# Performance work log

Hardware: AMD Instinct MI355X
Metric: run time of the kernel (lower is better)

The kernel has to match this reference:

```python
import jax, jax.numpy as jnp
import numpy as np

TEMP = 0.07  # softmax temperature T


def _l2norm(x, axis=1, eps=1e-12):
    return x / jnp.clip(jnp.linalg.norm(x, axis=axis, keepdims=True), eps, None)


def setup_inputs() -> dict:
    key = jax.random.key(0)
    k1, k2, k3, k4 = jax.random.split(key, 4)
    B, K, D = 256, 8192, 128
    q = jax.random.normal(k1, (B, D), dtype=jnp.float32)
    ba_queue = _l2norm(jax.random.normal(k2, (K, D), dtype=jnp.float32))
    nonba_queue = _l2norm(jax.random.normal(k3, (K, D), dtype=jnp.float32))
    targets = jax.random.randint(k4, (B,), 0, 2, dtype=jnp.int64)
    return {"q": q, "ba_queue": ba_queue, "nonba_queue": nonba_queue, "targets": targets}


def reference(q, ba_queue, nonba_queue, targets):
    K = ba_queue.shape[0]
    # encoder output is L2-normalized; queues are detached buffers
    qn = _l2norm(q, axis=1)
    all_feature = jnp.concatenate([qn, ba_queue, nonba_queue], axis=0)  # [N, D]
    all_label = jnp.concatenate([
        targets.astype(jnp.int32),
        jnp.ones((K,), dtype=jnp.int32),
        jnp.zeros((K,), dtype=jnp.int32),
    ])  # [N]
    N = all_feature.shape[0]

    # [N, N] similarity logits
    sim = jnp.matmul(all_feature, all_feature.T) / TEMP
    logits = sim - jax.lax.stop_gradient(jnp.max(sim, axis=1, keepdims=True))

    # positive mask (same label), excluding self
    mask = (all_label[:, None] == all_label[None, :]).astype(jnp.float32)
    logits_mask = 1.0 - jnp.eye(N, dtype=jnp.float32)
    mask = mask * logits_mask

    exp_logits = jnp.exp(logits) * logits_mask
    log_prob = logits - jnp.log(jnp.sum(exp_logits, axis=1, keepdims=True))
    mean_log_prob_pos = jnp.sum(mask * log_prob, axis=1) / jnp.sum(mask, axis=1)
    return -jnp.mean(mean_log_prob_pos)
```

## Files before the change

### kernel.cpp

```cpp
#include <hip/hip_runtime.h>
#include <hip/hip_bf16.h>
#include <stdint.h>

#define TEMPERATURE 0.07f
#define SC 20.6099312f

constexpr int NQ = 256;
constexpr int KQ = 8192;
constexpr int D  = 128;
constexpr int N  = NQ + 2 * KQ;
constexpr int CS = 26;
constexpr int BN = 128;
constexpr int NT = N / BN;
constexpr int RBM = N / 128;
constexpr int RBF = N / 256;

typedef float f32x16 __attribute__((ext_vector_type(16)));
typedef long  l64x2  __attribute__((ext_vector_type(2)));

constexpr size_t OFF_F32  = 0;
constexpr size_t OFF_8P   = OFF_F32  + (size_t)N * D * 4;
constexpr size_t OFF_8S   = OFF_8P   + (size_t)N * D;
constexpr size_t OFF_DIAG = OFF_8S   + (size_t)N * D;
constexpr size_t OFF_PART = OFF_DIAG + (size_t)N * 4;
constexpr size_t OFF_LP   = OFF_PART + (size_t)CS * N * 4;
constexpr size_t OFF_S    = OFF_LP   + (size_t)260 * 2 * 128 * 4;
constexpr size_t OFF_CNT  = OFF_S    + 2 * 128 * 4;
constexpr size_t OFF_BSUM = OFF_CNT  + 16;

__global__ __launch_bounds__(256) void k_prep(const float* __restrict__ q,
                                              const float* __restrict__ ba,
                                              const float* __restrict__ nb,
                                              const long long* __restrict__ tgt,
                                              float* __restrict__ ff,
                                              unsigned char* __restrict__ fb8p,
                                              unsigned char* __restrict__ fb8s,
                                              float* __restrict__ diag,
                                              float* __restrict__ lp) {
    __shared__ float red[4][2][128];
    int wid = threadIdx.x >> 6, lane = threadIdx.x & 63;
    int rbase = blockIdx.x * 64 + wid * 16;
    int slot = ((lane >> 2) & 1) * 4 + (lane >> 4);
    int poff = slot * 16 + ((lane >> 3) & 1) * 8 + (lane & 3) * 2;
    float s0x = 0.f, s0y = 0.f, s1x = 0.f, s1y = 0.f;
    for (int i = 0; i < 16; ++i) {
        int r = rbase + i;
        const float* src = (r < NQ) ? (q + (size_t)r * D)
                         : (r < NQ + KQ) ? (ba + (size_t)(r - NQ) * D)
                         : (nb + (size_t)(r - NQ - KQ) * D);
        float2 v = *(const float2*)(src + lane * 2);
        float a = v.x, b = v.y;
        int lab;
        if (r < NQ) {
            float ss = a * a + b * b;
            #pragma unroll
            for (int m = 1; m < 64; m <<= 1) ss += __shfl_xor(ss, m);
            float scale = 1.0f / fmaxf(sqrtf(ss), 1e-12f);
            a *= scale; b *= scale;
            lab = (int)tgt[r];
        } else {
            lab = (r < NQ + KQ) ? 1 : 0;
        }
        *(float2*)(ff + (size_t)r * D + lane * 2) = make_float2(a, b);
        int w8  = __builtin_amdgcn_cvt_pk_fp8_f32(a, b, 0, false);
        int w8s = __builtin_amdgcn_cvt_pk_fp8_f32(a * SC, b * SC, 0, false);
        *(unsigned short*)(fb8p + (size_t)r * D + poff)     = (unsigned short)w8;
        *(unsigned short*)(fb8s + (size_t)r * D + lane * 2) = (unsigned short)w8s;
        float dd = __builtin_amdgcn_cvt_f32_fp8(w8, 0) * __builtin_amdgcn_cvt_f32_fp8(w8s, 0)
                 + __builtin_amdgcn_cvt_f32_fp8(w8, 1) * __builtin_amdgcn_cvt_f32_fp8(w8s, 1);
        #pragma unroll
        for (int m = 1; m < 64; m <<= 1) dd += __shfl_xor(dd, m);
        if (lane == 0) diag[r] = __builtin_amdgcn_exp2f(dd - SC);
        if (lab) { s1x += a; s1y += b; } else { s0x += a; s0y += b; }
    }
    red[wid][0][lane * 2]     = s0x;
    red[wid][0][lane * 2 + 1] = s0y;
    red[wid][1][lane * 2]     = s1x;
    red[wid][1][lane * 2 + 1] = s1y;
    __syncthreads();
    int lab2 = threadIdx.x >> 7, d = threadIdx.x & 127;
    float s = red[0][lab2][d] + red[1][lab2][d] + red[2][lab2][d] + red[3][lab2][d];
    lp[((size_t)blockIdx.x * 2 + lab2) * 128 + d] = s;
}

__global__ __launch_bounds__(256) void k_lsum_b(const float* __restrict__ lp,
                                                const long long* __restrict__ tgt,
                                                float* __restrict__ S,
                                                int* __restrict__ cnt) {
    int lab = threadIdx.x >> 7;
    int d   = threadIdx.x & 127;
    float s[4] = {0.f, 0.f, 0.f, 0.f};
    for (int b = 0; b < 260; b += 4) {
        #pragma unroll
        for (int j = 0; j < 4; ++j)
            s[j] += lp[((size_t)(b + j) * 2 + lab) * 128 + d];
    }
    S[lab * 128 + d] = (s[0] + s[1]) + (s[2] + s[3]);
    if (threadIdx.x < 64) {
        int c = 0;
        #pragma unroll
        for (int i = 0; i < 4; ++i) c += (int)tgt[threadIdx.x + 64 * i];
        #pragma unroll
        for (int m = 1; m < 64; m <<= 1) c += __shfl_xor(c, m);
        if (threadIdx.x == 0) { cnt[0] = (NQ - c) + KQ; cnt[1] = c + KQ; }
    }
}

__global__ __launch_bounds__(256, 4) void k_main(const unsigned char* __restrict__ fb8p,
                                                 const unsigned char* __restrict__ fb8s,
                                                 float* __restrict__ part) {
    __shared__ __align__(16) unsigned char lds[2][BN * 128];
    const int bid = blockIdx.x;
    const int rb = bid / CS, cs = bid % CS;
    const int tid = threadIdx.x;
    const int lane = tid & 63;
    const int wid  = tid >> 6;
    const int l31 = lane & 31, lhi = lane >> 5;
    const int rw = rb * 128 + wid * 32;

    int soff[4], dstoff[4];
    #pragma unroll
    for (int i = 0; i < 4; ++i) {
        int crow = wid * 32 + i * 8 + (lane >> 3);
        soff[i]   = crow * 128 + (((lane & 7) ^ (crow & 7)) << 4);
        dstoff[i] = (wid * 4 + i) * 1024 + (lane & 63) * 16;
    }

    long rf[8];
    #pragma unroll
    for (int ks = 0; ks < 8; ++ks)
        rf[ks] = *(const long*)(fb8s + (size_t)(rw + l31) * D + ks * 16 + lhi * 8);

    float rsum = 0.f;

    {
        const unsigned char* base = fb8p + (size_t)cs * (BN * 128);
        #pragma unroll
        for (int i = 0; i < 4; ++i)
            __builtin_amdgcn_global_load_lds(
                (const __attribute__((address_space(1))) unsigned int*)(base + soff[i]),
                (__attribute__((address_space(3))) unsigned int*)(&lds[0][dstoff[i]]),
                16, 0, 0);
    }
    asm volatile("s_waitcnt vmcnt(0)" ::: "memory");
    __builtin_amdgcn_s_barrier();

    int cur = 0;
    for (int t = 0; t < 5; ++t) {
        int ct = cs + t * CS;

        if (t + 1 < 5) {
            const unsigned char* base = fb8p + ((size_t)ct + CS) * (BN * 128);
            #pragma unroll
            for (int i = 0; i < 4; ++i)
                __builtin_amdgcn_global_load_lds(
                    (const __attribute__((address_space(1))) unsigned int*)(base + soff[i]),
                    (__attribute__((address_space(3))) unsigned int*)(&lds[cur ^ 1][dstoff[i]]),
                    16, 0, 0);
        }

        f32x16 acc[4];
        #pragma unroll
        for (int i = 0; i < 4; ++i)
            #pragma unroll
            for (int e = 0; e < 16; ++e) acc[i][e] = -SC;

        __builtin_amdgcn_s_setprio(1);
        #pragma unroll
        for (int ks2 = 0; ks2 < 4; ++ks2) {
            #pragma unroll
            for (int cc = 0; cc < 4; ++cc) {
                int crow = cc * 32 + l31;
                l64x2 cf = *(const l64x2*)(&lds[cur][crow * 128 +
                               ((((lhi << 2) + ks2) ^ (crow & 7)) << 4)]);
                acc[cc] = __builtin_amdgcn_mfma_f32_32x32x16_fp8_fp8(cf.x, rf[ks2 * 2],     acc[cc], 0, 0, 0);
                acc[cc] = __builtin_amdgcn_mfma_f32_32x32x16_fp8_fp8(cf.y, rf[ks2 * 2 + 1], acc[cc], 0, 0, 0);
            }
        }
        __builtin_amdgcn_s_setprio(0);

        #pragma unroll
        for (int cc = 0; cc < 4; ++cc) {
            float p = 0.f;
            #pragma unroll
            for (int g = 0; g < 16; ++g)
                p += __builtin_amdgcn_exp2f(acc[cc][g]);
            rsum += p;
        }

        asm volatile("s_waitcnt vmcnt(0)" ::: "memory");
        __builtin_amdgcn_s_barrier();
        cur ^= 1;
    }

    rsum += __shfl_xor(rsum, 32);
    if (lane < 32)
        part[(size_t)cs * N + rw + lane] = rsum;
}

__global__ __launch_bounds__(256) void k_rowfin(const float* __restrict__ part,
                                                const float* __restrict__ ff,
                                                const float* __restrict__ S,
                                                const float* __restrict__ diag,
                                                const int* __restrict__ cnt,
                                                const long long* __restrict__ tgt,
                                                float* __restrict__ bsum) {
    __shared__ float sS[256];
    __shared__ float red[256];
    sS[threadIdx.x] = S[threadIdx.x];
    __syncthreads();
    int r = blockIdx.x * 256 + threadIdx.x;
    float se = 0.f;
    #pragma unroll
    for (int c = 0; c < CS; ++c) se += part[(size_t)c * N + r];
    se -= diag[r];
    float lse = logf(se) + 1.0f / TEMPERATURE;
    int lab = (r < NQ) ? (int)tgt[r] : ((r < NQ + KQ) ? 1 : 0);
    const float4* frow = (const float4*)(ff + (size_t)r * D);
    const float4* srow = (const float4*)(sS + lab * 128);
    float dS = 0.f;
    #pragma unroll
    for (int i = 0; i < 32; ++i) {
        float4 f = frow[i];
        float4 s = srow[i];
        dS += f.x * s.x + f.y * s.y + f.z * s.z + f.w * s.w;
    }
    float P = (float)(cnt[lab] - 1);
    float mlpp = (dS - 1.0f) / (TEMPERATURE * P) - lse;
    red[threadIdx.x] = mlpp;
    __syncthreads();
    for (int s2 = 128; s2 > 0; s2 >>= 1) {
        if (threadIdx.x < s2) red[threadIdx.x] += red[threadIdx.x + s2];
        __syncthreads();
    }
    if (threadIdx.x == 0) bsum[blockIdx.x] = red[0];
}

__global__ __launch_bounds__(64) void k_final(const float* __restrict__ bsum,
                                              float* __restrict__ out) {
    float s = bsum[threadIdx.x];
    if (threadIdx.x == 0) s += bsum[64];
    #pragma unroll
    for (int m = 1; m < 64; m <<= 1) s += __shfl_xor(s, m);
    if (threadIdx.x == 0) out[0] = -s / (float)N;
}

extern "C" void kernel_launch(void* const* d_in, const int* in_sizes, int n_in,
                              void* d_out, int out_size, void* d_ws, size_t ws_size,
                              hipStream_t stream) {
    const float* q       = (const float*)d_in[0];
    const float* ba      = (const float*)d_in[1];
    const float* nb      = (const float*)d_in[2];
    const long long* tgt = (const long long*)d_in[3];
    char* ws = (char*)d_ws;
    float*         ff   = (float*)(ws + OFF_F32);
    unsigned char* fb8p = (unsigned char*)(ws + OFF_8P);
    unsigned char* fb8s = (unsigned char*)(ws + OFF_8S);
    float*         diag = (float*)(ws + OFF_DIAG);
    float*         part = (float*)(ws + OFF_PART);
    float*         lp   = (float*)(ws + OFF_LP);
    float*         S    = (float*)(ws + OFF_S);
    int*           cnt  = (int*)(ws + OFF_CNT);
    float*         bsum = (float*)(ws + OFF_BSUM);

    k_prep  <<<260,      256, 0, stream>>>(q, ba, nb, tgt, ff, fb8p, fb8s, diag, lp);
    k_lsum_b<<<1,        256, 0, stream>>>(lp, tgt, S, cnt);
    k_main  <<<RBM * CS, 256, 0, stream>>>(fb8p, fb8s, part);
    k_rowfin<<<RBF,      256, 0, stream>>>(part, ff, S, diag, cnt, tgt, bsum);
    k_final <<<1,         64, 0, stream>>>(bsum, (float*)d_out);
}
```

Before: 96.21 us.

## Use scaled 32x32x64 f8f6f4 MFMA with new LDS swizzle and recompute diagonal

The main similarity kernel switches from pairs of 32x32x16 fp8 MFMAs to the gfx950 scaled 32x32x64 f8f6f4 MFMA with neutral scales, which halves the MFMA instruction count per tile. The LDS layout and swizzle change to match: the B operand is now stored row-major with a 16-slot XOR swizzle over 256-byte lines, and row fragments are loaded as 32-byte vectors. The fp8 self-similarity diagonal is no longer stored by the prep kernel and is instead recomputed in the row-finalize kernel from the fp32 features. The risk is LDS bank conflicts or register pressure under the new layout, plus the extra conversion work in k_rowfin.

Measured after the change: 80.21 us. -16.6%, faster.

```diff
diff --git a/kernel.cpp b/kernel.cpp
--- a/kernel.cpp
+++ b/kernel.cpp
@@ -16,13 +16,13 @@
 constexpr int RBF = N / 256;
 
 typedef float f32x16 __attribute__((ext_vector_type(16)));
-typedef long  l64x2  __attribute__((ext_vector_type(2)));
+typedef int   i32x4  __attribute__((ext_vector_type(4)));
+typedef int   i32x8  __attribute__((ext_vector_type(8)));
 
 constexpr size_t OFF_F32  = 0;
-constexpr size_t OFF_8P   = OFF_F32  + (size_t)N * D * 4;
-constexpr size_t OFF_8S   = OFF_8P   + (size_t)N * D;
-constexpr size_t OFF_DIAG = OFF_8S   + (size_t)N * D;
-constexpr size_t OFF_PART = OFF_DIAG + (size_t)N * 4;
+constexpr size_t OFF_8    = OFF_F32  + (size_t)N * D * 4;
+constexpr size_t OFF_8S   = OFF_8    + (size_t)N * D;
+constexpr size_t OFF_PART = OFF_8S   + (size_t)N * D;
 constexpr size_t OFF_LP   = OFF_PART + (size_t)CS * N * 4;
 constexpr size_t OFF_S    = OFF_LP   + (size_t)260 * 2 * 128 * 4;
 constexpr size_t OFF_CNT  = OFF_S    + 2 * 128 * 4;
@@ -33,15 +33,12 @@
                                               const float* __restrict__ nb,
                                               const long long* __restrict__ tgt,
                                               float* __restrict__ ff,
-                                              unsigned char* __restrict__ fb8p,
+                                              unsigned char* __restrict__ fb8,
                                               unsigned char* __restrict__ fb8s,
-                                              float* __restrict__ diag,
                                               float* __restrict__ lp) {
     __shared__ float red[4][2][128];
     int wid = threadIdx.x >> 6, lane = threadIdx.x & 63;
     int rbase = blockIdx.x * 64 + wid * 16;
-    int slot = ((lane >> 2) & 1) * 4 + (lane >> 4);
-    int poff = slot * 16 + ((lane >> 3) & 1) * 8 + (lane & 3) * 2;
     float s0x = 0.f, s0y = 0.f, s1x = 0.f, s1y = 0.f;
     for (int i = 0; i < 16; ++i) {
         int r = rbase + i;
@@ -64,13 +61,8 @@
         *(float2*)(ff + (size_t)r * D + lane * 2) = make_float2(a, b);
         int w8  = __builtin_amdgcn_cvt_pk_fp8_f32(a, b, 0, false);
         int w8s = __builtin_amdgcn_cvt_pk_fp8_f32(a * SC, b * SC, 0, false);
-        *(unsigned short*)(fb8p + (size_t)r * D + poff)     = (unsigned short)w8;
+        *(unsigned short*)(fb8  + (size_t)r * D + lane * 2) = (unsigned short)w8;
         *(unsigned short*)(fb8s + (size_t)r * D + lane * 2) = (unsigned short)w8s;
-        float dd = __builtin_amdgcn_cvt_f32_fp8(w8, 0) * __builtin_amdgcn_cvt_f32_fp8(w8s, 0)
-                 + __builtin_amdgcn_cvt_f32_fp8(w8, 1) * __builtin_amdgcn_cvt_f32_fp8(w8s, 1);
-        #pragma unroll
-        for (int m = 1; m < 64; m <<= 1) dd += __shfl_xor(dd, m);
-        if (lane == 0) diag[r] = __builtin_amdgcn_exp2f(dd - SC);
         if (lab) { s1x += a; s1y += b; } else { s0x += a; s0y += b; }
     }
     red[wid][0][lane * 2]     = s0x;
@@ -106,7 +98,7 @@
     }
 }
 
-__global__ __launch_bounds__(256, 4) void k_main(const unsigned char* __restrict__ fb8p,
+__global__ __launch_bounds__(256, 4) void k_main(const unsigned char* __restrict__ fb8,
                                                  const unsigned char* __restrict__ fb8s,
                                                  float* __restrict__ part) {
     __shared__ __align__(16) unsigned char lds[2][BN * 128];
@@ -118,28 +110,29 @@
     const int l31 = lane & 31, lhi = lane >> 5;
     const int rw = rb * 128 + wid * 32;
 
-    int soff[4], dstoff[4];
+    int soff[4];
     #pragma unroll
     for (int i = 0; i < 4; ++i) {
-        int crow = wid * 32 + i * 8 + (lane >> 3);
-        soff[i]   = crow * 128 + (((lane & 7) ^ (crow & 7)) << 4);
-        dstoff[i] = (wid * 4 + i) * 1024 + (lane & 63) * 16;
-    }
-
-    long rf[8];
-    #pragma unroll
-    for (int ks = 0; ks < 8; ++ks)
-        rf[ks] = *(const long*)(fb8s + (size_t)(rw + l31) * D + ks * 16 + lhi * 8);
+        int flat = i * 256 + tid;
+        int line = flat >> 4, p = flat & 15;
+        int pl = p ^ (line & 15);
+        soff[i] = (2 * line + (pl >> 3)) * 128 + (pl & 7) * 16;
+    }
+
+    i32x8 rf[2];
+    #pragma unroll
+    for (int s = 0; s < 2; ++s)
+        rf[s] = *(const i32x8*)(fb8s + (size_t)(rw + l31) * D + s * 64 + lhi * 32);
 
     float rsum = 0.f;
 
     {
-        const unsigned char* base = fb8p + (size_t)cs * (BN * 128);
+        const unsigned char* base = fb8 + (size_t)cs * (BN * 128);
         #pragma unroll
         for (int i = 0; i < 4; ++i)
             __builtin_amdgcn_global_load_lds(
                 (const __attribute__((address_space(1))) unsigned int*)(base + soff[i]),
-                (__attribute__((address_space(3))) unsigned int*)(&lds[0][dstoff[i]]),
+                (__attribute__((address_space(3))) unsigned int*)(&lds[0][(i * 256 + tid) * 16]),
                 16, 0, 0);
     }
     asm volatile("s_waitcnt vmcnt(0)" ::: "memory");
@@ -150,12 +143,12 @@
         int ct = cs + t * CS;
 
         if (t + 1 < 5) {
-            const unsigned char* base = fb8p + ((size_t)ct + CS) * (BN * 128);
+            const unsigned char* base = fb8 + ((size_t)ct + CS) * (BN * 128);
             #pragma unroll
             for (int i = 0; i < 4; ++i)
                 __builtin_amdgcn_global_load_lds(
                     (const __attribute__((address_space(1))) unsigned int*)(base + soff[i]),
-                    (__attribute__((address_space(3))) unsigned int*)(&lds[cur ^ 1][dstoff[i]]),
+                    (__attribute__((address_space(3))) unsigned int*)(&lds[cur ^ 1][(i * 256 + tid) * 16]),
                     16, 0, 0);
         }
 
@@ -167,14 +160,18 @@
 
         __builtin_amdgcn_s_setprio(1);
         #pragma unroll
-        for (int ks2 = 0; ks2 < 4; ++ks2) {
+        for (int s = 0; s < 2; ++s) {
             #pragma unroll
             for (int cc = 0; cc < 4; ++cc) {
                 int crow = cc * 32 + l31;
-                l64x2 cf = *(const l64x2*)(&lds[cur][crow * 128 +
-                               ((((lhi << 2) + ks2) ^ (crow & 7)) << 4)]);
-                acc[cc] = __builtin_amdgcn_mfma_f32_32x32x16_fp8_fp8(cf.x, rf[ks2 * 2],     acc[cc], 0, 0, 0);
-                acc[cc] = __builtin_amdgcn_mfma_f32_32x32x16_fp8_fp8(cf.y, rf[ks2 * 2 + 1], acc[cc], 0, 0, 0);
+                int line = crow >> 1;
+                int pb = ((crow & 1) << 3) + s * 4 + lhi * 2;
+                const unsigned char* lb = &lds[cur][line * 256];
+                i32x4 lo = *(const i32x4*)(lb + ((pb    ) ^ (line & 15)) * 16);
+                i32x4 hi = *(const i32x4*)(lb + ((pb + 1) ^ (line & 15)) * 16);
+                i32x8 a = {lo[0], lo[1], lo[2], lo[3], hi[0], hi[1], hi[2], hi[3]};
+                acc[cc] = __builtin_amdgcn_mfma_scale_f32_32x32x64_f8f6f4(
+                    a, rf[s], acc[cc], 0, 0, 0, 0x7f7f7f7f, 0, 0x7f7f7f7f);
             }
         }
         __builtin_amdgcn_s_setprio(0);
@@ -201,7 +198,6 @@
 __global__ __launch_bounds__(256) void k_rowfin(const float* __restrict__ part,
                                                 const float* __restrict__ ff,
                                                 const float* __restrict__ S,
-                                                const float* __restrict__ diag,
                                                 const int* __restrict__ cnt,
                                                 const long long* __restrict__ tgt,
                                                 float* __restrict__ bsum) {
@@ -213,18 +209,26 @@
     float se = 0.f;
     #pragma unroll
     for (int c = 0; c < CS; ++c) se += part[(size_t)c * N + r];
-    se -= diag[r];
-    float lse = logf(se) + 1.0f / TEMPERATURE;
     int lab = (r < NQ) ? (int)tgt[r] : ((r < NQ + KQ) ? 1 : 0);
     const float4* frow = (const float4*)(ff + (size_t)r * D);
     const float4* srow = (const float4*)(sS + lab * 128);
-    float dS = 0.f;
+    float dS = 0.f, dd = 0.f;
     #pragma unroll
     for (int i = 0; i < 32; ++i) {
         float4 f = frow[i];
         float4 s = srow[i];
         dS += f.x * s.x + f.y * s.y + f.z * s.z + f.w * s.w;
-    }
+        int wa  = __builtin_amdgcn_cvt_pk_fp8_f32(f.x, f.y, 0, false);
+        int wb  = __builtin_amdgcn_cvt_pk_fp8_f32(f.z, f.w, 0, false);
+        int wsa = __builtin_amdgcn_cvt_pk_fp8_f32(f.x * SC, f.y * SC, 0, false);
+        int wsb = __builtin_amdgcn_cvt_pk_fp8_f32(f.z * SC, f.w * SC, 0, false);
+        dd += __builtin_amdgcn_cvt_f32_fp8(wa, 0) * __builtin_amdgcn_cvt_f32_fp8(wsa, 0)
+            + __builtin_amdgcn_cvt_f32_fp8(wa, 1) * __builtin_amdgcn_cvt_f32_fp8(wsa, 1)
+            + __builtin_amdgcn_cvt_f32_fp8(wb, 0) * __builtin_amdgcn_cvt_f32_fp8(wsb, 0)
+            + __builtin_amdgcn_cvt_f32_fp8(wb, 1) * __builtin_amdgcn_cvt_f32_fp8(wsb, 1);
+    }
+    se -= __builtin_amdgcn_exp2f(dd - SC);
+    float lse = logf(se) + 1.0f / TEMPERATURE;
     float P = (float)(cnt[lab] - 1);
     float mlpp = (dS - 1.0f) / (TEMPERATURE * P) - lse;
     red[threadIdx.x] = mlpp;
@@ -254,18 +258,17 @@
     const long long* tgt = (const long long*)d_in[3];
     char* ws = (char*)d_ws;
     float*         ff   = (float*)(ws + OFF_F32);
-    unsigned char* fb8p = (unsigned char*)(ws + OFF_8P);
+    unsigned char* fb8  = (unsigned char*)(ws + OFF_8);
     unsigned char* fb8s = (unsigned char*)(ws + OFF_8S);
-    float*         diag = (float*)(ws + OFF_DIAG);
     float*         part = (float*)(ws + OFF_PART);
     float*         lp   = (float*)(ws + OFF_LP);
     float*         S    = (float*)(ws + OFF_S);
     int*           cnt  = (int*)(ws + OFF_CNT);
     float*         bsum = (float*)(ws + OFF_BSUM);
 
-    k_prep  <<<260,      256, 0, stream>>>(q, ba, nb, tgt, ff, fb8p, fb8s, diag, lp);
+    k_prep  <<<260,      256, 0, stream>>>(q, ba, nb, tgt, ff, fb8, fb8s, lp);
     k_lsum_b<<<1,        256, 0, stream>>>(lp, tgt, S, cnt);
-    k_main  <<<RBM * CS, 256, 0, stream>>>(fb8p, fb8s, part);
-    k_rowfin<<<RBF,      256, 0, stream>>>(part, ff, S, diag, cnt, tgt, bsum);
+    k_main  <<<RBM * CS, 256, 0, stream>>>(fb8, fb8s, part);
+    k_rowfin<<<RBF,      256, 0, stream>>>(part, ff, S, cnt, tgt, bsum);
     k_final <<<1,         64, 0, stream>>>(bsum, (float*)d_out);
 }
```
